# Performance work log

Measured on AMD Instinct MI355X. Metric: run time of the kernel, lower is better.

Reference implementation:

```python
import jax, jax.numpy as jnp
import numpy as np

B, N, HID, H, FFN, E = 1, 50000, 96, 8, 384, 800000
D = HID // H
SCALE = float(np.sqrt(D))


def _layernorm(x, g, b, eps=1e-5):
    mu = jnp.mean(x, axis=-1, keepdims=True)
    var = jnp.var(x, axis=-1, keepdims=True)
    return (x - mu) * jax.lax.rsqrt(var + eps) * g + b


def setup_inputs() -> dict:
    key = jax.random.key(0)
    ks = jax.random.split(key, 20)
    std = 0.02
    inp = {
        "x": jax.random.normal(ks[0], (B, N, HID), dtype=jnp.float32),
        "edge_index": jax.random.randint(ks[1], (2, E), 0, B * N, dtype=jnp.int32),
        "ln1_g": jnp.ones((HID,), jnp.float32),
        "ln1_b": jnp.zeros((HID,), jnp.float32),
        "Wq": jax.random.normal(ks[2], (HID, HID), jnp.float32) * std,
        "bq": jnp.zeros((HID,), jnp.float32),
        "Wk": jax.random.normal(ks[3], (HID, HID), jnp.float32) * std,
        "bk": jnp.zeros((HID,), jnp.float32),
        "Wv": jax.random.normal(ks[4], (HID, HID), jnp.float32) * std,
        "bv": jnp.zeros((HID,), jnp.float32),
        "Wo": jax.random.normal(ks[5], (HID, HID), jnp.float32) * std,
        "bo": jnp.zeros((HID,), jnp.float32),
        "ln2_g": jnp.ones((HID,), jnp.float32),
        "ln2_b": jnp.zeros((HID,), jnp.float32),
        "W1": jax.random.normal(ks[6], (HID, FFN), jnp.float32) * std,
        "b1": jnp.zeros((FFN,), jnp.float32),
        "W2": jax.random.normal(ks[7], (FFN, HID), jnp.float32) * std,
        "b2": jnp.zeros((HID,), jnp.float32),
    }
    return inp


def _sparse_attn(q, k, v, edge_index):
    # q,k,v: [B*N, H, D]; edge_index: [2, E]
    src_idx = edge_index[0].astype(jnp.int32)
    dst_idx = edge_index[1].astype(jnp.int32)
    src = k[src_idx]                                # [E, H, D]
    dest = q[dst_idx]                               # [E, H, D]
    score = jnp.sum(src * dest, axis=-1, keepdims=True) / SCALE  # [E, H, 1]
    score = jnp.exp(jnp.clip(score, -5.0, 5.0))
    msg = v[src_idx] * score                        # [E, H, D]
    wV = jax.ops.segment_sum(msg, dst_idx, num_segments=B * N)   # [B*N, H, D]
    Z = jax.ops.segment_sum(score, dst_idx, num_segments=B * N)  # [B*N, H, 1]
    return wV / (Z + 1e-6)


def reference(x, edge_index, ln1_g, ln1_b, Wq, bq, Wk, bk, Wv, bv, Wo, bo,
              ln2_g, ln2_b, W1, b1, W2, b2):
    # --- self-attention block ---
    y = _layernorm(x, ln1_g, ln1_b)                 # [B, N, HID]
    q = (y @ Wq + bq).reshape(B * N, H, D)
    k = (y @ Wk + bk).reshape(B * N, H, D)
    v = (y @ Wv + bv).reshape(B * N, H, D)
    a = _sparse_attn(q, k, v, edge_index)           # [B*N, H, D]
    a = a.reshape(B, N, HID)
    y = a @ Wo + bo
    x = x + y
    # --- FFN block ---
    y = _layernorm(x, ln2_g, ln2_b)
    y = jax.nn.gelu(y @ W1 + b1, approximate=False)
    y = y @ W2 + b2
    return x + y
```

## Files before the change

### kernel.cpp

```cpp
#include <hip/hip_runtime.h>
#include <hip/hip_bf16.h>
#include <math.h>

#define NN 50000
#define HIDD 96
#define NH 8
#define HD 12
#define FFND 384
#define NE 800000
#define NB 98
#define BSTRIDE 12288

#define INV_SCALE 0.28867513459481287f
#define LOG2E 1.4426950408889634f

typedef short short8 __attribute__((ext_vector_type(8)));
typedef float f32x4 __attribute__((ext_vector_type(4)));
typedef float f32x2 __attribute__((ext_vector_type(2)));

__device__ __forceinline__ float bf2f(unsigned short u) {
    union { unsigned int i; float f; } c;
    c.i = ((unsigned int)u) << 16;
    return c.f;
}

__global__ __launch_bounds__(256) void prep(
    int* __restrict__ gcursor,
    const float* __restrict__ Wq, const float* __restrict__ Wk,
    const float* __restrict__ Wv, const float* __restrict__ Wo,
    const float* __restrict__ W1, const float* __restrict__ W2,
    __hip_bfloat16* __restrict__ wbuf,
    const float* __restrict__ x, const float* __restrict__ g1,
    const float* __restrict__ b1, __hip_bfloat16* __restrict__ ybf) {
    int b = blockIdx.x;
    int t = threadIdx.x;
    if (b == 0) {
        if (t < 128) gcursor[t] = t * BSTRIDE;
        return;
    }
    if (b < 433) {
        int idx = b - 1;
        const float* W; __hip_bfloat16* D; int K, N; int i;
        if (idx < 144)      { W = W1; D = wbuf + 36864; K = 96;  N = 384; i = idx * 256 + t; }
        else if (idx < 288) { W = W2; D = wbuf + 73728; K = 384; N = 96;  i = (idx - 144) * 256 + t; }
        else {
            int slab = (idx - 288) / 36;
            W = (slab == 0) ? Wq : (slab == 1) ? Wk : (slab == 2) ? Wv : Wo;
            D = wbuf + slab * 9216; K = 96; N = 96;
            i = ((idx - 288) % 36) * 256 + t;
        }
        if (i < K * N) {
            int n = i / K, k = i % K;
            D[i] = __float2bfloat16(W[k * N + n]);
        }
    } else {
        int row = (b - 433) * 4 + (t >> 6);
        int lane = t & 63;
        if (row >= NN) return;
        const float* xr = x + (size_t)row * HIDD;
        float v0 = xr[lane];
        float v1 = (lane < 32) ? xr[64 + lane] : 0.0f;
        float s = v0 + v1, q = v0 * v0 + v1 * v1;
#pragma unroll
        for (int o = 32; o > 0; o >>= 1) {
            s += __shfl_xor(s, o);
            q += __shfl_xor(q, o);
        }
        float mean = s * (1.0f / 96.0f);
        float var = q * (1.0f / 96.0f) - mean * mean;
        float rs = rsqrtf(var + 1e-5f);
        __hip_bfloat16* yr = ybf + (size_t)row * HIDD;
        yr[lane] = __float2bfloat16((v0 - mean) * rs * g1[lane] + b1[lane]);
        if (lane < 32)
            yr[64 + lane] = __float2bfloat16((v1 - mean) * rs * g1[64 + lane] + b1[64 + lane]);
    }
}

template<int K, int EPI, int SMODE>
__device__ __forceinline__ void gemm_body(
    const __hip_bfloat16* __restrict__ A, const __hip_bfloat16* __restrict__ BT,
    const float* __restrict__ bias, const __hip_bfloat16* __restrict__ R,
    void* __restrict__ Cptr, int ldc, int col0, int koff, int xb) {
    constexpr int BK = (K > 192) ? 192 : K;
    __shared__ __hip_bfloat16 Bs[96][BK + 8];
    int t = threadIdx.x;
    int lane = t & 63, wave = t >> 6;
    int row0 = xb * 128 + wave * 32;
    int lr = lane & 15, kg = lane >> 4;
    bool val0 = (row0 + 16 <= NN);
    bool val1 = (row0 + 32 <= NN);
    int ra0 = val0 ? row0 : 0;
    int ra1 = val1 ? (row0 + 16) : 0;
    const __hip_bfloat16* A0 = A + (size_t)(ra0 + lr) * K + kg * 8;
    const __hip_bfloat16* A1 = A + (size_t)(ra1 + lr) * K + kg * 8;
    f32x4 acc[2][6];
#pragma unroll
    for (int f = 0; f < 2; f++)
#pragma unroll
        for (int ct = 0; ct < 6; ct++) acc[f][ct] = (f32x4){0.f, 0.f, 0.f, 0.f};

    for (int k0 = 0; k0 < K; k0 += BK) {
        for (int i = t * 8; i < 96 * BK; i += 256 * 8) {
            int r = i / BK, c = i % BK;
            *(short8*)&Bs[r][c] = *(const short8*)&BT[(size_t)r * K + k0 + c];
        }
        __syncthreads();
#pragma unroll
        for (int kc = 0; kc < BK; kc += 32) {
            short8 a0 = *(const short8*)(A0 + k0 + kc);
            short8 a1 = *(const short8*)(A1 + k0 + kc);
#pragma unroll
            for (int ct = 0; ct < 6; ct++) {
                short8 bf_ = *(const short8*)&Bs[ct * 16 + lr][kc + kg * 8];
                acc[0][ct] = __builtin_amdgcn_mfma_f32_16x16x32_bf16(a0, bf_, acc[0][ct], 0, 0, 0);
                acc[1][ct] = __builtin_amdgcn_mfma_f32_16x16x32_bf16(a1, bf_, acc[1][ct], 0, 0, 0);
            }
        }
        __syncthreads();
    }

#pragma unroll
    for (int f = 0; f < 2; f++) {
        if (f == 0 ? !val0 : !val1) continue;
        int crow = row0 + f * 16 + kg * 4;
#pragma unroll
        for (int ct = 0; ct < 6; ct++) {
            int col = col0 + ct * 16 + lr;
            float bb = bias[col];
#pragma unroll
            for (int r = 0; r < 4; r++) {
                float o = acc[f][ct][r] + bb;
                if (EPI == 1)
                    o = 0.5f * o * (1.0f + erff(o * 0.70710678118654752f));
                if (EPI == 2)
                    o += __bfloat162float(R[(size_t)(crow + r) * 96 + col]);
                if (SMODE == 0)
                    ((float*)Cptr)[(size_t)(crow + r) * ldc + col] = o;
                else if (SMODE == 1)
                    ((__hip_bfloat16*)Cptr)[(size_t)(crow + r) * ldc + col] = __float2bfloat16(o);
                else {
                    unsigned int enc = (unsigned int)__builtin_amdgcn_cvt_pk_fp8_f32(o, o, 0, false);
                    ((unsigned char*)Cptr)[(size_t)(crow + r) * 192 + ((col - col0) / 12) * 24 + koff + ((col - col0) % 12)]
                        = (unsigned char)(enc & 0xffu);
                }
            }
        }
    }
}

template<int K, int EPI, int SMODE>
__global__ __launch_bounds__(256) void mfma_gemm(
    const __hip_bfloat16* __restrict__ A, const __hip_bfloat16* __restrict__ BT,
    const float* __restrict__ bias, const __hip_bfloat16* __restrict__ R,
    void* __restrict__ Cptr, int ldc) {
    int col0 = blockIdx.y * 96;
    gemm_body<K, EPI, SMODE>(A, BT + (size_t)col0 * K, bias, R, Cptr, ldc, col0, 0, blockIdx.x);
}

__global__ __launch_bounds__(256) void scatter_qkv(
    const int* __restrict__ ei, int* __restrict__ gcursor,
    unsigned int* __restrict__ ebuf,
    const __hip_bfloat16* __restrict__ A, const __hip_bfloat16* __restrict__ wbuf,
    const float* __restrict__ bq, const float* __restrict__ bk,
    const float* __restrict__ bv,
    __hip_bfloat16* __restrict__ qbf, unsigned char* __restrict__ kv) {
    int b = blockIdx.x;
    if (b < 391) {
        __shared__ int lcount[128];
        __shared__ int lbase[128];
        int t = threadIdx.x;
        int e0 = b * 2048;
        if (t < 128) lcount[t] = 0;
        __syncthreads();
        int rank[8], dsts[8], srcv[8];
#pragma unroll
        for (int i = 0; i < 8; i++) {
            int e = e0 + t + i * 256;
            if (e < NE) {
                srcv[i] = ei[e];
                int d = ei[NE + e];
                dsts[i] = d;
                rank[i] = atomicAdd(&lcount[d >> 9], 1);
            } else dsts[i] = -1;
        }
        __syncthreads();
        if (t < 128) lbase[t] = lcount[t] ? atomicAdd(&gcursor[t], lcount[t]) : 0;
        __syncthreads();
#pragma unroll
        for (int i = 0; i < 8; i++) {
            if (dsts[i] >= 0) {
                int bk_ = dsts[i] >> 9;
                ebuf[lbase[bk_] + rank[i]] =
                    ((unsigned int)dsts[i] << 16) | (unsigned int)srcv[i];
            }
        }
    } else {
        int idx = b - 391;
        int y = idx / 391, xb = idx % 391;
        if (y == 0)
            gemm_body<96, 0, 1>(A, wbuf, bq, nullptr, qbf, 96, 0, 0, xb);
        else if (y == 1)
            gemm_body<96, 0, 2>(A, wbuf + 9216, bk, nullptr, kv, 0, 0, 0, xb);
        else
            gemm_body<96, 0, 2>(A, wbuf + 18432, bv, nullptr, kv, 0, 0, 12, xb);
    }
}

__global__ __launch_bounds__(1024) void bucket_build(
    const unsigned int* __restrict__ ebuf, const int* __restrict__ gcursor,
    uint2* __restrict__ rowrange, unsigned short* __restrict__ srcs) {
    __shared__ int cnt[512];
    int b = blockIdx.x;
    int t = threadIdx.x;
    int n0 = b * 512;
    int beg = b * BSTRIDE;
    int end = gcursor[b];
    if (t < 512) cnt[t] = 0;
    __syncthreads();
    for (int e = beg + t; e < end; e += 1024)
        atomicAdd(&cnt[(ebuf[e] >> 16) - n0], 1);
    __syncthreads();
    int my = (t < 512) ? cnt[t] : 0;
    for (int off = 1; off < 512; off <<= 1) {
        int v = (t >= off && t < 512) ? cnt[t - off] : 0;
        __syncthreads();
        if (t < 512) cnt[t] += v;
        __syncthreads();
    }
    int excl = (t > 0 && t < 512) ? cnt[t - 1] : 0;
    int base = beg + excl;
    if (t < 512 && n0 + t < NN)
        rowrange[n0 + t] = make_uint2((unsigned)base, (unsigned)(base + my));
    __syncthreads();
    if (t < 512) cnt[t] = base;
    __syncthreads();
    for (int e = beg + t; e < end; e += 1024) {
        unsigned int u = ebuf[e];
        int pos = atomicAdd(&cnt[(u >> 16) - n0], 1);
        srcs[pos] = (unsigned short)(u & 0xffffu);
    }
}

__global__ __launch_bounds__(256) void proj_ln(
    const __hip_bfloat16* __restrict__ A, const __hip_bfloat16* __restrict__ BT,
    const float* __restrict__ bias, const float* __restrict__ R,
    const float* __restrict__ g2, const float* __restrict__ b2v,
    __hip_bfloat16* __restrict__ x2, __hip_bfloat16* __restrict__ ybf) {
    constexpr int K = 96;
    __shared__ __hip_bfloat16 Bs[96][K + 8];
    int t = threadIdx.x;
    int lane = t & 63, wave = t >> 6;
    int row0 = blockIdx.x * 128 + wave * 32;
    int lr = lane & 15, kg = lane >> 4;
    bool val0 = (row0 + 16 <= NN);
    bool val1 = (row0 + 32 <= NN);
    int ra0 = val0 ? row0 : 0;
    int ra1 = val1 ? (row0 + 16) : 0;
    const __hip_bfloat16* A0 = A + (size_t)(ra0 + lr) * K + kg * 8;
    const __hip_bfloat16* A1 = A + (size_t)(ra1 + lr) * K + kg * 8;
    f32x4 acc[2][6];
#pragma unroll
    for (int f = 0; f < 2; f++)
#pragma unroll
        for (int ct = 0; ct < 6; ct++) acc[f][ct] = (f32x4){0.f, 0.f, 0.f, 0.f};

    for (int i = t * 8; i < 96 * K; i += 256 * 8) {
        int r = i / K, c = i % K;
        *(short8*)&Bs[r][c] = *(const short8*)&BT[(size_t)r * K + c];
    }
    __syncthreads();
#pragma unroll
    for (int kc = 0; kc < K; kc += 32) {
        short8 a0 = *(const short8*)(A0 + kc);
        short8 a1 = *(const short8*)(A1 + kc);
#pragma unroll
        for (int ct = 0; ct < 6; ct++) {
            short8 bf_ = *(const short8*)&Bs[ct * 16 + lr][kc + kg * 8];
            acc[0][ct] = __builtin_amdgcn_mfma_f32_16x16x32_bf16(a0, bf_, acc[0][ct], 0, 0, 0);
            acc[1][ct] = __builtin_amdgcn_mfma_f32_16x16x32_bf16(a1, bf_, acc[1][ct], 0, 0, 0);
        }
    }

    float bo_[6], gv[6], bv_[6];
#pragma unroll
    for (int ct = 0; ct < 6; ct++) {
        int col = ct * 16 + lr;
        bo_[ct] = bias[col];
        gv[ct]  = g2[col];
        bv_[ct] = b2v[col];
    }
#pragma unroll
    for (int f = 0; f < 2; f++) {
        if (f == 0 ? !val0 : !val1) continue;
        int crow = row0 + f * 16 + kg * 4;
#pragma unroll
        for (int r = 0; r < 4; r++) {
            int row = crow + r;
            float o[6], s1 = 0.f, s2 = 0.f;
#pragma unroll
            for (int ct = 0; ct < 6; ct++) {
                int col = ct * 16 + lr;
                float val = acc[f][ct][r] + bo_[ct] + R[(size_t)row * 96 + col];
                o[ct] = val; s1 += val; s2 += val * val;
            }
#pragma unroll
            for (int m = 1; m < 16; m <<= 1) {
                s1 += __shfl_xor(s1, m);
                s2 += __shfl_xor(s2, m);
            }
            float mu = s1 * (1.0f / 96.0f);
            float var = s2 * (1.0f / 96.0f) - mu * mu;
            float rs = rsqrtf(var + 1e-5f);
#pragma unroll
            for (int ct = 0; ct < 6; ct++) {
                int col = ct * 16 + lr;
                x2[(size_t)row * 96 + col] = __float2bfloat16(o[ct]);
                ybf[(size_t)row * 96 + col] =
                    __float2bfloat16((o[ct] - mu) * rs * gv[ct] + bv_[ct]);
            }
        }
    }
}

__global__ __launch_bounds__(256) void attn_gather(
    const __hip_bfloat16* __restrict__ qbf, const unsigned char* __restrict__ kv,
    const uint2* __restrict__ rowrange, const unsigned short* __restrict__ srcs,
    __hip_bfloat16* __restrict__ abf) {
    int wave = (blockIdx.x * blockDim.x + threadIdx.x) >> 6;
    int lane = threadIdx.x & 63;
    if (wave >= NN) return;
    int dst = wave;
    int h = lane & 7;
    int eslot = lane >> 3;
    float qf[12];
    {
        const uint2* qp = (const uint2*)(qbf + (size_t)dst * HIDD + h * HD);
        uint2 u0 = qp[0], u1 = qp[1], u2 = qp[2];
        unsigned int w[6] = {u0.x, u0.y, u1.x, u1.y, u2.x, u2.y};
#pragma unroll
        for (int i = 0; i < 6; i++) {
            qf[2 * i]     = bf2f((unsigned short)(w[i] & 0xffffu));
            qf[2 * i + 1] = bf2f((unsigned short)(w[i] >> 16));
        }
    }
    uint2 rr = rowrange[dst];
    int beg = (int)rr.x, end = (int)rr.y;
    float acc[12];
#pragma unroll
    for (int i = 0; i < 12; i++) acc[i] = 0.0f;
    float zz = 0.0f;

    int e = beg + eslot;
    bool has = e < end;
    uint2 cA, cB, cC;
    if (has) {
        int src = (int)srcs[e];
        const uint2* kp = (const uint2*)(kv + (size_t)src * 192 + h * 24);
        cA = kp[0]; cB = kp[1]; cC = kp[2];
    }
    while (has) {
        int en = e + 8;
        bool hasn = en < end;
        uint2 nA, nB, nC;
        if (hasn) {
            int srcn = (int)srcs[en];
            const uint2* kp = (const uint2*)(kv + (size_t)srcn * 192 + h * 24);
            nA = kp[0]; nB = kp[1]; nC = kp[2];
        }
        f32x2 p;
        float dot = 0.0f;
        p = __builtin_amdgcn_cvt_pk_f32_fp8(cA.x, false); dot += p[0] * qf[0]  + p[1] * qf[1];
        p = __builtin_amdgcn_cvt_pk_f32_fp8(cA.x, true);  dot += p[0] * qf[2]  + p[1] * qf[3];
        p = __builtin_amdgcn_cvt_pk_f32_fp8(cA.y, false); dot += p[0] * qf[4]  + p[1] * qf[5];
        p = __builtin_amdgcn_cvt_pk_f32_fp8(cA.y, true);  dot += p[0] * qf[6]  + p[1] * qf[7];
        p = __builtin_amdgcn_cvt_pk_f32_fp8(cB.x, false); dot += p[0] * qf[8]  + p[1] * qf[9];
        p = __builtin_amdgcn_cvt_pk_f32_fp8(cB.x, true);  dot += p[0] * qf[10] + p[1] * qf[11];
        float s = fminf(fmaxf(dot * INV_SCALE, -5.0f), 5.0f);
        float sc = exp2f(s * LOG2E);
        p = __builtin_amdgcn_cvt_pk_f32_fp8(cB.y, false); acc[0]  += p[0] * sc; acc[1]  += p[1] * sc;
        p = __builtin_amdgcn_cvt_pk_f32_fp8(cB.y, true);  acc[2]  += p[0] * sc; acc[3]  += p[1] * sc;
        p = __builtin_amdgcn_cvt_pk_f32_fp8(cC.x, false); acc[4]  += p[0] * sc; acc[5]  += p[1] * sc;
        p = __builtin_amdgcn_cvt_pk_f32_fp8(cC.x, true);  acc[6]  += p[0] * sc; acc[7]  += p[1] * sc;
        p = __builtin_amdgcn_cvt_pk_f32_fp8(cC.y, false); acc[8]  += p[0] * sc; acc[9]  += p[1] * sc;
        p = __builtin_amdgcn_cvt_pk_f32_fp8(cC.y, true);  acc[10] += p[0] * sc; acc[11] += p[1] * sc;
        zz += sc;
        cA = nA; cB = nB; cC = nC;
        e = en; has = hasn;
    }
#pragma unroll
    for (int m = 8; m < 64; m <<= 1) {
#pragma unroll
        for (int i = 0; i < 12; i++) acc[i] += __shfl_xor(acc[i], m);
        zz += __shfl_xor(zz, m);
    }
    if (eslot == 0) {
        float inv = 1.0f / (zz + 1e-6f);
        __hip_bfloat16* ar = abf + (size_t)dst * HIDD + h * HD;
#pragma unroll
        for (int i = 0; i < 12; i++) ar[i] = __float2bfloat16(acc[i] * inv);
    }
}

extern "C" void kernel_launch(void* const* d_in, const int* in_sizes, int n_in,
                              void* d_out, int out_size, void* d_ws, size_t ws_size,
                              hipStream_t stream) {
    const float* x     = (const float*)d_in[0];
    const int*   ei    = (const int*)d_in[1];
    const float* ln1_g = (const float*)d_in[2];
    const float* ln1_b = (const float*)d_in[3];
    const float* Wq    = (const float*)d_in[4];
    const float* bq    = (const float*)d_in[5];
    const float* Wk    = (const float*)d_in[6];
    const float* bk    = (const float*)d_in[7];
    const float* Wv    = (const float*)d_in[8];
    const float* bv    = (const float*)d_in[9];
    const float* Wo    = (const float*)d_in[10];
    const float* bo    = (const float*)d_in[11];
    const float* ln2_g = (const float*)d_in[12];
    const float* ln2_b = (const float*)d_in[13];
    const float* W1    = (const float*)d_in[14];
    const float* b1    = (const float*)d_in[15];
    const float* W2    = (const float*)d_in[16];
    const float* b2    = (const float*)d_in[17];
    float* out = (float*)d_out;

    float* ws = (float*)d_ws;
    const size_t NF = (size_t)NN * HIDD;
    __hip_bfloat16* qbf = (__hip_bfloat16*)ws;
    unsigned char*  kv  = (unsigned char*)(ws + NF / 2);
    __hip_bfloat16* abf = (__hip_bfloat16*)(ws + NF / 2 + NF);
    __hip_bfloat16* hbf = (__hip_bfloat16*)ws;
    __hip_bfloat16* x2  = (__hip_bfloat16*)(ws + 2 * NF);
    __hip_bfloat16* ybf = (__hip_bfloat16*)(ws + 2 * NF + NF / 2);
    int* ibase = (int*)(ws + 3 * NF);
    uint2* rowrange = (uint2*)ibase;
    unsigned short* srcs = (unsigned short*)(ibase + 2 * NN);
    int* gcursor = ibase + 2 * NN + (NB * BSTRIDE + 1) / 2;
    unsigned int* ebuf = (unsigned int*)(gcursor + 128);
    __hip_bfloat16* wbuf = (__hip_bfloat16*)(ws + 3 * NF + NF / 2);
    __hip_bfloat16* WoT = wbuf + 27648;
    __hip_bfloat16* W1T = wbuf + 36864;
    __hip_bfloat16* W2T = wbuf + 73728;

    const int MT = (NN + 127) / 128;

    prep<<<433 + 12500, 256, 0, stream>>>(gcursor, Wq, Wk, Wv, Wo, W1, W2, wbuf,
                                          x, ln1_g, ln1_b, ybf);
    scatter_qkv<<<391 + 3 * MT, 256, 0, stream>>>(ei, gcursor, ebuf,
                                                  ybf, wbuf, bq, bk, bv, qbf, kv);
    bucket_build<<<NB, 1024, 0, stream>>>(ebuf, gcursor, rowrange, srcs);
    attn_gather<<<(NN + 3) / 4, 256, 0, stream>>>(qbf, kv, rowrange, srcs, abf);
    proj_ln<<<MT, 256, 0, stream>>>(abf, WoT, bo, x, ln2_g, ln2_b, x2, ybf);
    {
        dim3 g(MT, 4);
        mfma_gemm<96, 1, 1><<<g, 256, 0, stream>>>(ybf, W1T, b1, nullptr, hbf, FFND);
    }
    mfma_gemm<384, 2, 0><<<MT, 256, 0, stream>>>(hbf, W2T, b2, x2, out, 96);
}
```

Measured before the change: 142.9 us.

## Fuse FFN up and down GEMMs into one kernel with LDS-resident hidden

Replaces the two separate FFN GEMM launches with a single kernel. Each 64-row block computes the GELU hidden activations into shared memory and immediately multiplies them by W2, adding bias and residual. This removes the global write and re-read of the 50000x384 bf16 hidden tensor and one launch. In exchange it uses about 70KB of LDS per block, which limits occupancy. Weight tiles are also reloaded per block with unpipelined syncs.

```diff
diff --git a/kernel.cpp b/kernel.cpp
--- a/kernel.cpp
+++ b/kernel.cpp
@@ -148,15 +148,6 @@
     }
 }
 
-template<int K, int EPI, int SMODE>
-__global__ __launch_bounds__(256) void mfma_gemm(
-    const __hip_bfloat16* __restrict__ A, const __hip_bfloat16* __restrict__ BT,
-    const float* __restrict__ bias, const __hip_bfloat16* __restrict__ R,
-    void* __restrict__ Cptr, int ldc) {
-    int col0 = blockIdx.y * 96;
-    gemm_body<K, EPI, SMODE>(A, BT + (size_t)col0 * K, bias, R, Cptr, ldc, col0, 0, blockIdx.x);
-}
-
 __global__ __launch_bounds__(256) void scatter_qkv(
     const int* __restrict__ ei, int* __restrict__ gcursor,
     unsigned int* __restrict__ ebuf,
@@ -317,6 +308,93 @@
                 x2[(size_t)row * 96 + col] = __float2bfloat16(o[ct]);
                 ybf[(size_t)row * 96 + col] =
                     __float2bfloat16((o[ct] - mu) * rs * gv[ct] + bv_[ct]);
+            }
+        }
+    }
+}
+
+__global__ __launch_bounds__(256) void ffn_fused(
+    const __hip_bfloat16* __restrict__ ybf, const __hip_bfloat16* __restrict__ W1T,
+    const __hip_bfloat16* __restrict__ W2T, const float* __restrict__ b1,
+    const float* __restrict__ b2v, const __hip_bfloat16* __restrict__ x2,
+    float* __restrict__ out) {
+    __shared__ __hip_bfloat16 hlds[64][392];
+    __shared__ __hip_bfloat16 Bs[96][104];
+    int t = threadIdx.x, lane = t & 63, wave = t >> 6;
+    int row0 = blockIdx.x * 64;
+    int lr = lane & 15, kg = lane >> 4;
+    int rw = row0 + wave * 16;
+    bool valid = (rw + 16 <= NN);
+    int ra = valid ? rw : 0;
+
+    short8 af[3];
+#pragma unroll
+    for (int kc = 0; kc < 3; kc++)
+        af[kc] = *(const short8*)&ybf[(size_t)(ra + lr) * 96 + kc * 32 + kg * 8];
+
+    for (int s = 0; s < 4; s++) {
+        for (int i = t * 8; i < 96 * 96; i += 256 * 8) {
+            int r = i / 96, c = i % 96;
+            *(short8*)&Bs[r][c] = *(const short8*)&W1T[(size_t)(s * 96 + r) * 96 + c];
+        }
+        __syncthreads();
+        f32x4 acc[6];
+#pragma unroll
+        for (int ct = 0; ct < 6; ct++) acc[ct] = (f32x4){0.f, 0.f, 0.f, 0.f};
+#pragma unroll
+        for (int kc = 0; kc < 3; kc++) {
+#pragma unroll
+            for (int ct = 0; ct < 6; ct++) {
+                short8 bf_ = *(const short8*)&Bs[ct * 16 + lr][kc * 32 + kg * 8];
+                acc[ct] = __builtin_amdgcn_mfma_f32_16x16x32_bf16(af[kc], bf_, acc[ct], 0, 0, 0);
+            }
+        }
+#pragma unroll
+        for (int ct = 0; ct < 6; ct++) {
+            int col = s * 96 + ct * 16 + lr;
+            float bb = b1[col];
+#pragma unroll
+            for (int r = 0; r < 4; r++) {
+                float o = acc[ct][r] + bb;
+                o = 0.5f * o * (1.0f + erff(o * 0.70710678118654752f));
+                hlds[wave * 16 + kg * 4 + r][col] = __float2bfloat16(o);
+            }
+        }
+        __syncthreads();
+    }
+
+    f32x4 acc2[6];
+#pragma unroll
+    for (int ct = 0; ct < 6; ct++) acc2[ct] = (f32x4){0.f, 0.f, 0.f, 0.f};
+    for (int c = 0; c < 4; c++) {
+        for (int i = t * 8; i < 96 * 96; i += 256 * 8) {
+            int r = i / 96, cc = i % 96;
+            *(short8*)&Bs[r][cc] = *(const short8*)&W2T[(size_t)r * 384 + c * 96 + cc];
+        }
+        __syncthreads();
+#pragma unroll
+        for (int kc = 0; kc < 3; kc++) {
+            short8 a = *(const short8*)&hlds[wave * 16 + lr][c * 96 + kc * 32 + kg * 8];
+#pragma unroll
+            for (int ct = 0; ct < 6; ct++) {
+                short8 bf_ = *(const short8*)&Bs[ct * 16 + lr][kc * 32 + kg * 8];
+                acc2[ct] = __builtin_amdgcn_mfma_f32_16x16x32_bf16(a, bf_, acc2[ct], 0, 0, 0);
+            }
+        }
+        __syncthreads();
+    }
+
+    if (valid) {
+        int crow = rw + kg * 4;
+#pragma unroll
+        for (int ct = 0; ct < 6; ct++) {
+            int col = ct * 16 + lr;
+            float bb = b2v[col];
+#pragma unroll
+            for (int r = 0; r < 4; r++) {
+                float o = acc2[ct][r] + bb
+                        + __bfloat162float(x2[(size_t)(crow + r) * 96 + col]);
+                out[(size_t)(crow + r) * 96 + col] = o;
             }
         }
     }
@@ -429,7 +507,6 @@
     __hip_bfloat16* qbf = (__hip_bfloat16*)ws;
     unsigned char*  kv  = (unsigned char*)(ws + NF / 2);
     __hip_bfloat16* abf = (__hip_bfloat16*)(ws + NF / 2 + NF);
-    __hip_bfloat16* hbf = (__hip_bfloat16*)ws;
     __hip_bfloat16* x2  = (__hip_bfloat16*)(ws + 2 * NF);
     __hip_bfloat16* ybf = (__hip_bfloat16*)(ws + 2 * NF + NF / 2);
     int* ibase = (int*)(ws + 3 * NF);
@@ -443,6 +520,7 @@
     __hip_bfloat16* W2T = wbuf + 73728;
 
     const int MT = (NN + 127) / 128;
+    const int FT = (NN + 63) / 64;
 
     prep<<<433 + 12500, 256, 0, stream>>>(gcursor, Wq, Wk, Wv, Wo, W1, W2, wbuf,
                                           x, ln1_g, ln1_b, ybf);
@@ -451,9 +529,5 @@
     bucket_build<<<NB, 1024, 0, stream>>>(ebuf, gcursor, rowrange, srcs);
     attn_gather<<<(NN + 3) / 4, 256, 0, stream>>>(qbf, kv, rowrange, srcs, abf);
     proj_ln<<<MT, 256, 0, stream>>>(abf, WoT, bo, x, ln2_g, ln2_b, x2, ybf);
-    {
-        dim3 g(MT, 4);
-        mfma_gemm<96, 1, 1><<<g, 256, 0, stream>>>(ybf, W1T, b1, nullptr, hbf, FFND);
-    }
-    mfma_gemm<384, 2, 0><<<MT, 256, 0, stream>>>(hbf, W2T, b2, x2, out, 96);
-}
+    ffn_fused<<<FT, 256, 0, stream>>>(ybf, W1T, W2T, b1, b2, x2, out);
+}
```

Result: no change. 143.1 us (+0.1%).
